# Kernel optimization log

Measured on AMD Instinct MI355X. Metric: run time of the kernel, lower is better.

Reference implementation:

```python
import jax, jax.numpy as jnp
import numpy as np

T, D, I, E, K = 2048, 768, 2048, 8, 2


def setup_inputs() -> dict:
    key = jax.random.key(0)
    ks = jax.random.split(key, 9)
    x = jax.random.normal(ks[0], (T, D), jnp.float32)
    router_weight = jax.random.normal(ks[1], (E, D), jnp.float32) * 0.02
    shared_w_gate = jax.random.normal(ks[2], (I, D), jnp.float32) * 0.02
    shared_w_up = jax.random.normal(ks[3], (I, D), jnp.float32) * 0.02
    shared_w_down = jax.random.normal(ks[4], (D, I), jnp.float32) * 0.02
    # ternary quantized expert weights in {-1, 0, 1}
    expert_q_gate = jax.random.randint(ks[5], (E, I, D), 0, 3, jnp.int32) - 1
    expert_q_up = jax.random.randint(ks[6], (E, I, D), 0, 3, jnp.int32) - 1
    expert_q_down = jax.random.randint(ks[7], (E, D, I), 0, 3, jnp.int32) - 1
    # per-expert, per-matrix dequant scales (gate, up, down)
    expert_scales = jax.random.uniform(ks[8], (E, 3), jnp.float32) * 0.05 + 0.01
    return {
        "x": x,
        "router_weight": router_weight,
        "shared_w_gate": shared_w_gate,
        "shared_w_up": shared_w_up,
        "shared_w_down": shared_w_down,
        "expert_q_gate": expert_q_gate,
        "expert_q_up": expert_q_up,
        "expert_q_down": expert_q_down,
        "expert_scales": expert_scales,
        "top_k": K,
    }


def _swiglu(x, wg, wu, wd):
    # down( silu(gate(x)) * up(x) )
    return (jax.nn.silu(x @ wg.T) * (x @ wu.T)) @ wd.T


def reference(x, router_weight, shared_w_gate, shared_w_up, shared_w_down,
              expert_q_gate, expert_q_up, expert_q_down, expert_scales, top_k):
    # --- router: softmax -> top-k -> renormalize ---
    probs = jax.nn.softmax(x @ router_weight.T, axis=-1)            # [T, E]
    vals, idx = jax.lax.top_k(probs, top_k)                          # [T, K]
    vals = vals / jnp.sum(vals, axis=-1, keepdims=True)
    n_experts = router_weight.shape[0]
    # combine weights as dense [T, E] gate (one-hot scatter of top-k probs)
    gate = jnp.sum(jax.nn.one_hot(idx, n_experts, dtype=x.dtype) * vals[..., None], axis=1)

    # --- dequantize paged ternary experts: w = ternary * scale ---
    wg = expert_q_gate.astype(x.dtype) * expert_scales[:, 0, None, None]  # [E, I, D]
    wu = expert_q_up.astype(x.dtype) * expert_scales[:, 1, None, None]    # [E, I, D]
    wd = expert_q_down.astype(x.dtype) * expert_scales[:, 2, None, None]  # [E, D, I]

    # --- expert SwiGLU, computed per expert and combined with the gate ---
    h = jax.nn.silu(jnp.einsum('td,eid->tei', x, wg)) * jnp.einsum('td,eid->tei', x, wu)
    expert_out = jnp.einsum('tei,edi->ted', h, wd)                   # [T, E, D]
    moe_out = jnp.einsum('te,ted->td', gate, expert_out)             # [T, D]

    # --- always-on shared expert ---
    shared_out = _swiglu(x, shared_w_gate, shared_w_up, shared_w_down)
    return shared_out + moe_out
```

## Files before the change

kernel.cpp:

```cpp
#include <hip/hip_runtime.h>
#include <hip/hip_bf16.h>

#define TDIM 2048
#define DDIM 768
#define IDIM 2048
#define NEXP 8

typedef __bf16 v8bf __attribute__((ext_vector_type(8)));
typedef __bf16 v4bf __attribute__((ext_vector_type(4)));
typedef float v4f __attribute__((ext_vector_type(4)));
typedef int   v4i __attribute__((ext_vector_type(4)));
typedef float v4ff __attribute__((ext_vector_type(4)));

#define MFMA_B16(A,B,C) __builtin_amdgcn_mfma_f32_16x16x32_bf16(A,B,C,0,0,0)

typedef __attribute__((address_space(1))) const unsigned int* gas_t;
typedef __attribute__((address_space(3))) unsigned int* las_t;

__device__ __forceinline__ void gload16(const void* g, void* l) {
  __builtin_amdgcn_global_load_lds((gas_t)g, (las_t)l, 16, 0, 0);
}

__device__ __forceinline__ v4bf conv4(v4i r, int isint) {
  v4bf v;
  if (isint) {
    v[0] = (__bf16)(float)r[0]; v[1] = (__bf16)(float)r[1];
    v[2] = (__bf16)(float)r[2]; v[3] = (__bf16)(float)r[3];
  } else {
    v[0] = (__bf16)__int_as_float(r[0]); v[1] = (__bf16)__int_as_float(r[1]);
    v[2] = (__bf16)__int_as_float(r[2]); v[3] = (__bf16)__int_as_float(r[3]);
  }
  return v;
}

__global__ __launch_bounds__(256)
void prep_kernel(const float* __restrict__ x, const float* __restrict__ rw,
                 const float* __restrict__ es, __hip_bfloat16* __restrict__ xb,
                 int* __restrict__ cnt, int* __restrict__ lists, float* __restrict__ wt)
{
  const int b = blockIdx.x;
  const int tid = threadIdx.x;

  if (b < 512) {
    const int t = b * 4 + (tid >> 6);
    const int lane = tid & 63;
    const float* xp = x + (size_t)t * DDIM;
    float4 xv0 = *(const float4*)(xp + lane * 4);
    float4 xv1 = *(const float4*)(xp + 256 + lane * 4);
    float4 xv2 = *(const float4*)(xp + 512 + lane * 4);
    float logit[NEXP];
#pragma unroll
    for (int e = 0; e < NEXP; ++e) {
      const float* w = rw + (size_t)e * DDIM;
      float4 w0 = *(const float4*)(w + lane * 4);
      float4 w1 = *(const float4*)(w + 256 + lane * 4);
      float4 w2 = *(const float4*)(w + 512 + lane * 4);
      float p = xv0.x * w0.x + xv0.y * w0.y + xv0.z * w0.z + xv0.w * w0.w
              + xv1.x * w1.x + xv1.y * w1.y + xv1.z * w1.z + xv1.w * w1.w
              + xv2.x * w2.x + xv2.y * w2.y + xv2.z * w2.z + xv2.w * w2.w;
#pragma unroll
      for (int off = 32; off > 0; off >>= 1) p += __shfl_down(p, off, 64);
      logit[e] = p;
    }
    if (lane == 0) {
      float m = logit[0];
#pragma unroll
      for (int e = 1; e < NEXP; ++e) m = fmaxf(m, logit[e]);
      float pr[NEXP];
#pragma unroll
      for (int e = 0; e < NEXP; ++e) pr[e] = expf(logit[e] - m);
      int i0 = 0; float v0 = pr[0];
#pragma unroll
      for (int e = 1; e < NEXP; ++e) if (pr[e] > v0) { v0 = pr[e]; i0 = e; }
      int i1 = -1; float v1 = -1.f;
#pragma unroll
      for (int e = 0; e < NEXP; ++e) if (e != i0 && pr[e] > v1) { v1 = pr[e]; i1 = e; }
      float inv = 1.f / (v0 + v1);
      int p0 = atomicAdd(&cnt[i0], 1);
      lists[i0 * TDIM + p0] = t * 2;
      wt[t * 2] = v0 * inv * es[i0 * 3 + 2];
      int p1 = atomicAdd(&cnt[i1], 1);
      lists[i1 * TDIM + p1] = t * 2 + 1;
      wt[t * 2 + 1] = v1 * inv * es[i1 * 3 + 2];
    }
    return;
  }

  const int lc = tid & 31;
  const int rowloc = tid >> 5;
  const int row = (b - 512) * 8 + rowloc;
  const float* sp = x + (size_t)row * DDIM;
  __hip_bfloat16* dp = xb + (size_t)row * DDIM;
  v4ff r[6];
#pragma unroll
  for (int i = 0; i < 6; ++i) r[i] = *(const v4ff*)(sp + (lc + i * 32) * 4);
#pragma unroll
  for (int i = 0; i < 6; ++i) {
    v4bf v;
    v[0] = (__bf16)r[i][0]; v[1] = (__bf16)r[i][1];
    v[2] = (__bf16)r[i][2]; v[3] = (__bf16)r[i][3];
    *(v4bf*)(dp + (lc + i * 32) * 4) = v;
  }
}

__global__ __launch_bounds__(256)
void gu_gemm_kernel(const __hip_bfloat16* __restrict__ xb,
                    const int* __restrict__ qg, const int* __restrict__ qu,
                    const float* __restrict__ sgw, const float* __restrict__ suw,
                    const float* __restrict__ es,
                    const int* __restrict__ cnt, const int* __restrict__ lists,
                    __hip_bfloat16* __restrict__ h)
{
  const int b = blockIdx.x;
  int tm, tn, count, isint;
  const char *srcG, *srcU;
  const int* listE = nullptr;
  float sgc, suc;
  if (b < 4096) {
    const int e = b >> 9; tm = (b >> 5) & 15; tn = b & 31;
    count = cnt[e];
    if (tm * 128 >= count) return;
    srcG = (const char*)(qg + (size_t)e * IDIM * DDIM);
    srcU = (const char*)(qu + (size_t)e * IDIM * DDIM);
    listE = lists + e * TDIM;
    sgc = es[e * 3 + 0]; suc = es[e * 3 + 1];
    isint = 1;
  } else {
    const int b2 = b - 4096; tm = b2 >> 5; tn = b2 & 31;
    count = TDIM;
    srcG = (const char*)sgw; srcU = (const char*)suw;
    sgc = 1.f; suc = 1.f; isint = 0;
  }

  __shared__ __align__(16) char As[2][16384];
  __shared__ __align__(16) char Bs[16384];

  const int tid = threadIdx.x;
  const int lane = tid & 63;
  const int wid = tid >> 6;
  const int wr = wid >> 1, wc = wid & 1;
  const int lr16 = lane & 15, hk = lane >> 4;

  const int cA = (((lane & 7) ^ (lane >> 3)) << 4);
  const char* aptr[4];
#pragma unroll
  for (int p = 0; p < 4; ++p) {
    const int row = p * 32 + wid * 8 + (lane >> 3);
    const int rg = tm * 128 + row;
    int tok;
    if (listE) { const int idx = rg < count ? rg : count - 1; tok = listE[idx] >> 1; }
    else tok = rg;
    aptr[p] = (const char*)xb + (size_t)tok * (DDIM * 2) + cA;
  }

  const int lanec = tid & 15;
  const int rowb = tid >> 4;
  const char* bq[8];
  int dsoff[8];
#pragma unroll
  for (int p = 0; p < 8; ++p) {
    const int srcrow = (tn * 4 + (p >> 1)) * 16 + rowb;
    const char* base = (p & 1) ? srcU : srcG;
    bq[p] = base + ((size_t)srcrow * DDIM + lanec * 4) * 4;
    const int r = rowb + 16 * p;
    dsoff[p] = r * 128 + ((lanec * 8) ^ ((rowb & 7) << 4));
  }

  v4f acc[4][4] = {};
  v4i braw[8];
  v4bf bconv[8];

#pragma unroll
  for (int p = 0; p < 4; ++p) gload16(aptr[p], As[0] + wid * 1024 + p * 4096);
#pragma unroll
  for (int p = 0; p < 8; ++p) braw[p] = *(const v4i*)(bq[p]);
#pragma unroll
  for (int p = 0; p < 8; ++p) bconv[p] = conv4(braw[p], isint);

  for (int kt = 0; kt < 12; ++kt) {
    const int cur = kt & 1;
#pragma unroll
    for (int p = 0; p < 8; ++p) *(v4bf*)(Bs + dsoff[p]) = bconv[p];
    __syncthreads();
    if (kt + 1 < 12) {
#pragma unroll
      for (int p = 0; p < 4; ++p) gload16(aptr[p] + (kt + 1) * 128, As[cur ^ 1] + wid * 1024 + p * 4096);
#pragma unroll
      for (int p = 0; p < 8; ++p) braw[p] = *(const v4i*)(bq[p] + (kt + 1) * 256);
    }
#pragma unroll
    for (int ks = 0; ks < 2; ++ks) {
      const int colb = ks * 64 + hk * 16;
      v8bf fa[4], fb[4];
#pragma unroll
      for (int m = 0; m < 4; ++m) {
        const int r = wr * 64 + m * 16 + lr16;
        fa[m] = *(const v8bf*)(As[cur] + r * 128 + (colb ^ ((r & 7) << 4)));
      }
#pragma unroll
      for (int n = 0; n < 4; ++n) {
        const int r = wc * 64 + n * 16 + lr16;
        fb[n] = *(const v8bf*)(Bs + r * 128 + (colb ^ ((r & 7) << 4)));
      }
#pragma unroll
      for (int n = 0; n < 4; ++n)
#pragma unroll
        for (int m = 0; m < 4; ++m) acc[m][n] = MFMA_B16(fa[m], fb[n], acc[m][n]);
    }
    __syncthreads();
    if (kt + 1 < 12) {
#pragma unroll
      for (int p = 0; p < 8; ++p) bconv[p] = conv4(braw[p], isint);
    }
  }

#pragma unroll
  for (int m = 0; m < 4; ++m) {
#pragma unroll
    for (int j = 0; j < 4; ++j) {
      const int rl = wr * 64 + m * 16 + hk * 4 + j;
      const int rg = tm * 128 + rl;
      if (rg >= count) continue;
      const size_t drow = listE ? (size_t)listE[rg] : (size_t)(4096 + rg);
      __hip_bfloat16* dh = h + drow * IDIM + (tn * 4 + wc * 2) * 16 + lr16;
#pragma unroll
      for (int p = 0; p < 2; ++p) {
        const float g = acc[m][2 * p][j] * sgc;
        const float u = acc[m][2 * p + 1][j] * suc;
        dh[p * 16] = __float2bfloat16(g / (1.f + __expf(-g)) * u);
      }
    }
  }
}

__global__ __launch_bounds__(256)
void down_gemm_kernel(const __hip_bfloat16* __restrict__ h,
                      const int* __restrict__ qd, const float* __restrict__ sdw,
                      const float* __restrict__ wt,
                      const int* __restrict__ cnt, const int* __restrict__ lists,
                      float* __restrict__ part)
{
  const int b = blockIdx.x;
  int tm, tn, count, isint;
  const char* srcB;
  const int* listE = nullptr;
  if (b < 768) {
    const int e = b / 96; const int r = b % 96; tm = r / 6; tn = r % 6;
    count = cnt[e];
    if (tm * 128 >= count) return;
    srcB = (const char*)(qd + (size_t)e * DDIM * IDIM);
    listE = lists + e * TDIM;
    isint = 1;
  } else {
    const int r = b - 768; tm = r / 6; tn = r % 6;
    count = TDIM;
    srcB = (const char*)sdw;
    isint = 0;
  }

  __shared__ __align__(16) char As[2][16384];
  __shared__ __align__(16) char Bs[16384];

  const int tid = threadIdx.x;
  const int lane = tid & 63;
  const int wid = tid >> 6;
  const int wr = wid >> 1, wc = wid & 1;
  const int lr16 = lane & 15, hk = lane >> 4;

  const int cA = (((lane & 7) ^ (lane >> 3)) << 4);
  const char* aptr[4];
#pragma unroll
  for (int p = 0; p < 4; ++p) {
    const int row = p * 32 + wid * 8 + (lane >> 3);
    const int rg = tm * 128 + row;
    int srow;
    if (listE) { const int idx = rg < count ? rg : count - 1; srow = listE[idx]; }
    else srow = 4096 + rg;
    aptr[p] = (const char*)h + (size_t)srow * (IDIM * 2) + cA;
  }

  const int lanec = tid & 15;
  const int rowb = tid >> 4;
  const char* bq[8];
  int dsoff[8];
#pragma unroll
  for (int p = 0; p < 8; ++p) {
    const int srcrow = tn * 128 + rowb + 16 * p;
    bq[p] = srcB + ((size_t)srcrow * IDIM + lanec * 4) * 4;
    const int r = rowb + 16 * p;
    dsoff[p] = r * 128 + ((lanec * 8) ^ ((rowb & 7) << 4));
  }

  v4f acc[4][4] = {};
  v4i braw[8];
  v4bf bconv[8];

#pragma unroll
  for (int p = 0; p < 4; ++p) gload16(aptr[p], As[0] + wid * 1024 + p * 4096);
#pragma unroll
  for (int p = 0; p < 8; ++p) braw[p] = *(const v4i*)(bq[p]);
#pragma unroll
  for (int p = 0; p < 8; ++p) bconv[p] = conv4(braw[p], isint);

  for (int kt = 0; kt < 32; ++kt) {
    const int cur = kt & 1;
#pragma unroll
    for (int p = 0; p < 8; ++p) *(v4bf*)(Bs + dsoff[p]) = bconv[p];
    __syncthreads();
    if (kt + 1 < 32) {
#pragma unroll
      for (int p = 0; p < 4; ++p) gload16(aptr[p] + (kt + 1) * 128, As[cur ^ 1] + wid * 1024 + p * 4096);
#pragma unroll
      for (int p = 0; p < 8; ++p) braw[p] = *(const v4i*)(bq[p] + (kt + 1) * 256);
    }
#pragma unroll
    for (int ks = 0; ks < 2; ++ks) {
      const int colb = ks * 64 + hk * 16;
      v8bf fa[4], fb[4];
#pragma unroll
      for (int m = 0; m < 4; ++m) {
        const int r = wr * 64 + m * 16 + lr16;
        fa[m] = *(const v8bf*)(As[cur] + r * 128 + (colb ^ ((r & 7) << 4)));
      }
#pragma unroll
      for (int n = 0; n < 4; ++n) {
        const int r = wc * 64 + n * 16 + lr16;
        fb[n] = *(const v8bf*)(Bs + r * 128 + (colb ^ ((r & 7) << 4)));
      }
#pragma unroll
      for (int n = 0; n < 4; ++n)
#pragma unroll
        for (int m = 0; m < 4; ++m) acc[m][n] = MFMA_B16(fa[m], fb[n], acc[m][n]);
    }
    __syncthreads();
    if (kt + 1 < 32) {
#pragma unroll
      for (int p = 0; p < 8; ++p) bconv[p] = conv4(braw[p], isint);
    }
  }

#pragma unroll
  for (int m = 0; m < 4; ++m) {
#pragma unroll
    for (int j = 0; j < 4; ++j) {
      const int rl = wr * 64 + m * 16 + hk * 4 + j;
      const int rg = tm * 128 + rl;
      if (rg >= count) continue;
      int orow; float w;
      if (listE) { const int slot = listE[rg]; orow = slot; w = wt[slot]; }
      else { orow = 4096 + rg; w = 1.f; }
      float* dst = part + (size_t)orow * DDIM + tn * 128 + wc * 64 + lr16;
#pragma unroll
      for (int n = 0; n < 4; ++n) dst[n * 16] = acc[m][n][j] * w;
    }
  }
}

__global__ __launch_bounds__(256)
void combine_kernel(const float* __restrict__ part, float* __restrict__ out)
{
  const int i4 = blockIdx.x * 256 + threadIdx.x;
  const int i0 = i4 * 4;
  const int t = i0 / DDIM;
  const int d = i0 - t * DDIM;
  float4 a = *(const float4*)(part + (size_t)(2 * t) * DDIM + d);
  float4 bb = *(const float4*)(part + (size_t)(2 * t + 1) * DDIM + d);
  float4 c = *(const float4*)(part + (size_t)(4096 + t) * DDIM + d);
  float4 r;
  r.x = a.x + bb.x + c.x;
  r.y = a.y + bb.y + c.y;
  r.z = a.z + bb.z + c.z;
  r.w = a.w + bb.w + c.w;
  *(float4*)(out + i0) = r;
}

extern "C" void kernel_launch(void* const* d_in, const int* in_sizes, int n_in,
                              void* d_out, int out_size, void* d_ws, size_t ws_size,
                              hipStream_t stream)
{
  const float* x   = (const float*)d_in[0];
  const float* rw  = (const float*)d_in[1];
  const float* swg = (const float*)d_in[2];
  const float* swu = (const float*)d_in[3];
  const float* swd = (const float*)d_in[4];
  const int*   qg  = (const int*)d_in[5];
  const int*   qu  = (const int*)d_in[6];
  const int*   qd  = (const int*)d_in[7];
  const float* es  = (const float*)d_in[8];
  float* out = (float*)d_out;

  char* ws = (char*)d_ws;
  size_t off = 0;
  auto alloc = [&](size_t bytes) { void* p = ws + off; off = (off + bytes + 255) & ~(size_t)255; return p; };
  int*   cnt   = (int*)alloc(NEXP * 4);
  int*   lists = (int*)alloc((size_t)NEXP * TDIM * 4);
  float* wt    = (float*)alloc((size_t)2 * TDIM * 4);
  __hip_bfloat16* xb = (__hip_bfloat16*)alloc((size_t)TDIM * DDIM * 2);
  __hip_bfloat16* h  = (__hip_bfloat16*)alloc((size_t)(4096 + TDIM) * IDIM * 2);
  float* part = (float*)alloc((size_t)(4096 + TDIM) * DDIM * 4);

  hipMemsetAsync(cnt, 0, NEXP * 4, stream);

  prep_kernel<<<768, 256, 0, stream>>>(x, rw, es, xb, cnt, lists, wt);
  gu_gemm_kernel<<<4096 + 512, 256, 0, stream>>>(xb, qg, qu, swg, swu, es, cnt, lists, h);
  down_gemm_kernel<<<768 + 96, 256, 0, stream>>>(h, qd, swd, wt, cnt, lists, part);
  combine_kernel<<<(TDIM * DDIM / 4) / 256, 256, 0, stream>>>(part, out);
}
```

Baseline: 389.1 us.

## Pre-convert down-projection weights to bf16 inside gate/up kernel, stream via LDS loads

Adds extra blocks to the gate/up GEMM launch that convert all expert int32 and shared fp32 down-projection weights to bf16 buffers in workspace. The down GEMM then loads the B tiles directly into LDS with global_load_lds instead of loading 4-byte values into registers and converting them. It drops the A-side double buffering and adds a 3-blocks-per-CU launch bound to raise occupancy. The trade is that every expert's down weights are converted, even inactive ones, which adds a write and a re-read of about 28 MB. The single-buffered loop also loses load/compute overlap within a block.

Measured after the change: 369.1 us. 1.05x faster.

```diff
diff --git a/kernel.cpp b/kernel.cpp
--- a/kernel.cpp
+++ b/kernel.cpp
@@ -32,6 +32,17 @@
   }
   return v;
 }
+__device__ __forceinline__ v4bf cvt4_i(v4i a) {
+  v4bf v;
+  v[0] = (__bf16)(float)a[0]; v[1] = (__bf16)(float)a[1];
+  v[2] = (__bf16)(float)a[2]; v[3] = (__bf16)(float)a[3];
+  return v;
+}
+__device__ __forceinline__ v4bf cvt4_f(v4ff a) {
+  v4bf v;
+  v[0] = (__bf16)a[0]; v[1] = (__bf16)a[1]; v[2] = (__bf16)a[2]; v[3] = (__bf16)a[3];
+  return v;
+}
 
 __global__ __launch_bounds__(256)
 void prep_kernel(const float* __restrict__ x, const float* __restrict__ rw,
@@ -95,23 +106,62 @@
 #pragma unroll
   for (int i = 0; i < 6; ++i) r[i] = *(const v4ff*)(sp + (lc + i * 32) * 4);
 #pragma unroll
-  for (int i = 0; i < 6; ++i) {
-    v4bf v;
-    v[0] = (__bf16)r[i][0]; v[1] = (__bf16)r[i][1];
-    v[2] = (__bf16)r[i][2]; v[3] = (__bf16)r[i][3];
-    *(v4bf*)(dp + (lc + i * 32) * 4) = v;
-  }
+  for (int i = 0; i < 6; ++i) *(v4bf*)(dp + (lc + i * 32) * 4) = cvt4_f(r[i]);
 }
 
 __global__ __launch_bounds__(256)
-void gu_gemm_kernel(const __hip_bfloat16* __restrict__ xb,
-                    const int* __restrict__ qg, const int* __restrict__ qu,
-                    const float* __restrict__ sgw, const float* __restrict__ suw,
-                    const float* __restrict__ es,
-                    const int* __restrict__ cnt, const int* __restrict__ lists,
-                    __hip_bfloat16* __restrict__ h)
+void gu_fused_kernel(const __hip_bfloat16* __restrict__ xb,
+                     const int* __restrict__ qg, const int* __restrict__ qu,
+                     const float* __restrict__ sgw, const float* __restrict__ suw,
+                     const int* __restrict__ qd, const float* __restrict__ sdw,
+                     const float* __restrict__ es,
+                     const int* __restrict__ cnt, const int* __restrict__ lists,
+                     __hip_bfloat16* __restrict__ h,
+                     __hip_bfloat16* __restrict__ wdb, __hip_bfloat16* __restrict__ sdb)
 {
   const int b = blockIdx.x;
+  const int tid = threadIdx.x;
+
+  if (b >= 4608) {
+    const int pb = b - 4608;
+    const int lc = tid & 31;
+    const int rowloc = tid >> 5;
+    const int* isrc = nullptr; const float* fsrc = nullptr;
+    __hip_bfloat16* dstT; int r8, isint;
+    if (pb < 768) {
+      const int e = pb / 96; r8 = pb % 96;
+      isrc = qd + (size_t)e * DDIM * IDIM;
+      dstT = wdb + (size_t)e * DDIM * IDIM;
+      isint = 1;
+    } else {
+      r8 = pb - 768;
+      fsrc = sdw;
+      dstT = sdb;
+      isint = 0;
+    }
+    const int srcrow = r8 * 8 + rowloc;
+    __hip_bfloat16* dp = dstT + (size_t)srcrow * IDIM;
+#pragma unroll
+    for (int h2 = 0; h2 < 2; ++h2) {
+      if (isint) {
+        const v4i* sp = (const v4i*)(isrc + (size_t)srcrow * IDIM);
+        v4i r[8];
+#pragma unroll
+        for (int j = 0; j < 8; ++j) r[j] = sp[lc + (h2 * 8 + j) * 32];
+#pragma unroll
+        for (int j = 0; j < 8; ++j) *(v4bf*)(dp + (lc + (h2 * 8 + j) * 32) * 4) = cvt4_i(r[j]);
+      } else {
+        const v4ff* sp = (const v4ff*)(fsrc + (size_t)srcrow * IDIM);
+        v4ff r[8];
+#pragma unroll
+        for (int j = 0; j < 8; ++j) r[j] = sp[lc + (h2 * 8 + j) * 32];
+#pragma unroll
+        for (int j = 0; j < 8; ++j) *(v4bf*)(dp + (lc + (h2 * 8 + j) * 32) * 4) = cvt4_f(r[j]);
+      }
+    }
+    return;
+  }
+
   int tm, tn, count, isint;
   const char *srcG, *srcU;
   const int* listE = nullptr;
@@ -135,7 +185,6 @@
   __shared__ __align__(16) char As[2][16384];
   __shared__ __align__(16) char Bs[16384];
 
-  const int tid = threadIdx.x;
   const int lane = tid & 63;
   const int wid = tid >> 6;
   const int wr = wid >> 1, wc = wid & 1;
@@ -233,32 +282,30 @@
   }
 }
 
-__global__ __launch_bounds__(256)
+__global__ __launch_bounds__(256, 3)
 void down_gemm_kernel(const __hip_bfloat16* __restrict__ h,
-                      const int* __restrict__ qd, const float* __restrict__ sdw,
+                      const __hip_bfloat16* __restrict__ wdb, const __hip_bfloat16* __restrict__ sdb,
                       const float* __restrict__ wt,
                       const int* __restrict__ cnt, const int* __restrict__ lists,
                       float* __restrict__ part)
 {
   const int b = blockIdx.x;
-  int tm, tn, count, isint;
-  const char* srcB;
+  int tm, tn, count;
+  const char* bbase;
   const int* listE = nullptr;
   if (b < 768) {
     const int e = b / 96; const int r = b % 96; tm = r / 6; tn = r % 6;
     count = cnt[e];
     if (tm * 128 >= count) return;
-    srcB = (const char*)(qd + (size_t)e * DDIM * IDIM);
+    bbase = (const char*)(wdb + (size_t)e * DDIM * IDIM);
     listE = lists + e * TDIM;
-    isint = 1;
   } else {
     const int r = b - 768; tm = r / 6; tn = r % 6;
     count = TDIM;
-    srcB = (const char*)sdw;
-    isint = 0;
-  }
-
-  __shared__ __align__(16) char As[2][16384];
+    bbase = (const char*)sdb;
+  }
+
+  __shared__ __align__(16) char As[16384];
   __shared__ __align__(16) char Bs[16384];
 
   const int tid = threadIdx.x;
@@ -269,6 +316,7 @@
 
   const int cA = (((lane & 7) ^ (lane >> 3)) << 4);
   const char* aptr[4];
+  const char* bptr[4];
 #pragma unroll
   for (int p = 0; p < 4; ++p) {
     const int row = p * 32 + wid * 8 + (lane >> 3);
@@ -277,42 +325,17 @@
     if (listE) { const int idx = rg < count ? rg : count - 1; srow = listE[idx]; }
     else srow = 4096 + rg;
     aptr[p] = (const char*)h + (size_t)srow * (IDIM * 2) + cA;
-  }
-
-  const int lanec = tid & 15;
-  const int rowb = tid >> 4;
-  const char* bq[8];
-  int dsoff[8];
-#pragma unroll
-  for (int p = 0; p < 8; ++p) {
-    const int srcrow = tn * 128 + rowb + 16 * p;
-    bq[p] = srcB + ((size_t)srcrow * IDIM + lanec * 4) * 4;
-    const int r = rowb + 16 * p;
-    dsoff[p] = r * 128 + ((lanec * 8) ^ ((rowb & 7) << 4));
+    bptr[p] = bbase + (size_t)(tn * 128 + row) * (IDIM * 2) + cA;
   }
 
   v4f acc[4][4] = {};
-  v4i braw[8];
-  v4bf bconv[8];
-
-#pragma unroll
-  for (int p = 0; p < 4; ++p) gload16(aptr[p], As[0] + wid * 1024 + p * 4096);
-#pragma unroll
-  for (int p = 0; p < 8; ++p) braw[p] = *(const v4i*)(bq[p]);
-#pragma unroll
-  for (int p = 0; p < 8; ++p) bconv[p] = conv4(braw[p], isint);
 
   for (int kt = 0; kt < 32; ++kt) {
-    const int cur = kt & 1;
-#pragma unroll
-    for (int p = 0; p < 8; ++p) *(v4bf*)(Bs + dsoff[p]) = bconv[p];
+#pragma unroll
+    for (int p = 0; p < 4; ++p) gload16(aptr[p] + kt * 128, As + wid * 1024 + p * 4096);
+#pragma unroll
+    for (int p = 0; p < 4; ++p) gload16(bptr[p] + kt * 128, Bs + wid * 1024 + p * 4096);
     __syncthreads();
-    if (kt + 1 < 32) {
-#pragma unroll
-      for (int p = 0; p < 4; ++p) gload16(aptr[p] + (kt + 1) * 128, As[cur ^ 1] + wid * 1024 + p * 4096);
-#pragma unroll
-      for (int p = 0; p < 8; ++p) braw[p] = *(const v4i*)(bq[p] + (kt + 1) * 256);
-    }
 #pragma unroll
     for (int ks = 0; ks < 2; ++ks) {
       const int colb = ks * 64 + hk * 16;
@@ -320,7 +343,7 @@
 #pragma unroll
       for (int m = 0; m < 4; ++m) {
         const int r = wr * 64 + m * 16 + lr16;
-        fa[m] = *(const v8bf*)(As[cur] + r * 128 + (colb ^ ((r & 7) << 4)));
+        fa[m] = *(const v8bf*)(As + r * 128 + (colb ^ ((r & 7) << 4)));
       }
 #pragma unroll
       for (int n = 0; n < 4; ++n) {
@@ -333,10 +356,6 @@
         for (int m = 0; m < 4; ++m) acc[m][n] = MFMA_B16(fa[m], fb[n], acc[m][n]);
     }
     __syncthreads();
-    if (kt + 1 < 32) {
-#pragma unroll
-      for (int p = 0; p < 8; ++p) bconv[p] = conv4(braw[p], isint);
-    }
   }
 
 #pragma unroll
@@ -395,14 +414,17 @@
   int*   cnt   = (int*)alloc(NEXP * 4);
   int*   lists = (int*)alloc((size_t)NEXP * TDIM * 4);
   float* wt    = (float*)alloc((size_t)2 * TDIM * 4);
-  __hip_bfloat16* xb = (__hip_bfloat16*)alloc((size_t)TDIM * DDIM * 2);
-  __hip_bfloat16* h  = (__hip_bfloat16*)alloc((size_t)(4096 + TDIM) * IDIM * 2);
+  __hip_bfloat16* xb  = (__hip_bfloat16*)alloc((size_t)TDIM * DDIM * 2);
+  __hip_bfloat16* wdb = (__hip_bfloat16*)alloc((size_t)NEXP * DDIM * IDIM * 2);
+  __hip_bfloat16* sdb = (__hip_bfloat16*)alloc((size_t)DDIM * IDIM * 2);
+  __hip_bfloat16* h   = (__hip_bfloat16*)alloc((size_t)(4096 + TDIM) * IDIM * 2);
   float* part = (float*)alloc((size_t)(4096 + TDIM) * DDIM * 4);
 
   hipMemsetAsync(cnt, 0, NEXP * 4, stream);
 
   prep_kernel<<<768, 256, 0, stream>>>(x, rw, es, xb, cnt, lists, wt);
-  gu_gemm_kernel<<<4096 + 512, 256, 0, stream>>>(xb, qg, qu, swg, swu, es, cnt, lists, h);
-  down_gemm_kernel<<<768 + 96, 256, 0, stream>>>(h, qd, swd, wt, cnt, lists, part);
+  gu_fused_kernel<<<4608 + 864, 256, 0, stream>>>(xb, qg, qu, swg, swu, qd, swd, es,
+                                                  cnt, lists, h, wdb, sdb);
+  down_gemm_kernel<<<768 + 96, 256, 0, stream>>>(h, wdb, sdb, wt, cnt, lists, part);
   combine_kernel<<<(TDIM * DDIM / 4) / 256, 256, 0, stream>>>(part, out);
 }
```
